# Performance work log

Hardware: AMD Instinct MI355X
Metric: run time of the kernel (lower is better)

The kernel has to match this reference:

```python
import jax, jax.numpy as jnp
import numpy as np

B, D, G, P = 4, 768, 64, 256
H = 12
HD = D // H
SCALE = HD ** -0.5


def setup_inputs() -> dict:
    key = jax.random.key(0)
    k1, k2, k3, k4 = jax.random.split(key, 4)
    x = jax.random.normal(k1, (B, D, G, P), dtype=jnp.float32)
    # per-group patch-patch mask; p=0.9 keep so no row is fully masked in practice
    mask = jax.random.bernoulli(k2, 0.9, (G, P, P))
    w_qkv = jax.random.normal(k3, (3 * D, D), dtype=jnp.float32) * (D ** -0.5)
    w_proj = jax.random.normal(k4, (D, D), dtype=jnp.float32) * (D ** -0.5)
    b_proj = jnp.zeros((D,), dtype=jnp.float32)
    return {"x": x, "mask": mask, "w_qkv": w_qkv, "w_proj": w_proj, "b_proj": b_proj}


def reference(x, mask, w_qkv, w_proj, b_proj):
    # 1x1 conv == channel matmul: [B,D,G,P] -> [B,3D,G,P]
    qkv = jnp.einsum('bdgp,ed->begp', x, w_qkv)
    # channel layout is (qkv, head, head_dim)
    qkv = qkv.reshape(B, 3, H, HD, G, P)
    qkv = jnp.transpose(qkv, (1, 0, 2, 4, 5, 3))  # [3, B, H, G, P, HD]
    q, k, v = qkv[0], qkv[1], qkv[2]
    attn = jnp.einsum('bhgpd,bhgqd->bhgpq', q, k) * SCALE  # [B,H,G,P,P]
    mask_value = -jnp.finfo(attn.dtype).max
    attn = jnp.where(mask[None, None], attn, mask_value)
    attn = jax.nn.softmax(attn, axis=-1)
    out = jnp.einsum('bhgpq,bhgqd->bhgpd', attn, v)  # [B,H,G,P,HD]
    out = jnp.transpose(out, (0, 1, 4, 2, 3)).reshape(B, D, G, P)
    out = jnp.einsum('bdgp,ed->begp', out, w_proj) + b_proj[None, :, None, None]
    return out
```

## Files before the change

### kernel.cpp

```cpp
#include <hip/hip_runtime.h>
#include <float.h>

#define D_    768
#define GD    64
#define PD    256
#define HH    12
#define HDD   64
#define NGP   (GD*PD)
#define SCALE 0.125f

typedef __bf16 bf16x8 __attribute__((ext_vector_type(8)));
typedef __bf16 bf16x4 __attribute__((ext_vector_type(4)));
typedef _Float16 f16x8 __attribute__((ext_vector_type(8)));
typedef _Float16 f16x4 __attribute__((ext_vector_type(4)));
typedef float  f32x4  __attribute__((ext_vector_type(4)));

__device__ __forceinline__ void gload_lds16(const __bf16* g, __bf16* l) {
  __builtin_amdgcn_global_load_lds(
      (const __attribute__((address_space(1))) void*)g,
      (__attribute__((address_space(3))) void*)l, 16, 0, 0);
}

__device__ __forceinline__ unsigned short f2bf_bits(float f) {
  __bf16 h = (__bf16)f;
  unsigned short u;
  __builtin_memcpy(&u, &h, 2);
  return u;
}

__global__ void wcast_k(const float* __restrict__ in, __bf16* __restrict__ out, int n) {
  int i = (blockIdx.x * 256 + threadIdx.x) * 4;
  if (i >= n) return;
  float4 v = *(const float4*)(in + i);
  bf16x4 o;
  o[0] = (__bf16)v.x; o[1] = (__bf16)v.y; o[2] = (__bf16)v.z; o[3] = (__bf16)v.w;
  *(bf16x4*)(out + i) = o;
}

__global__ void tcast_k(const float* __restrict__ in, __bf16* __restrict__ out) {
  __shared__ float s[32][66];
  const int tid = threadIdx.x;
  const int c0 = blockIdx.x * 64;
  const int r0 = blockIdx.y * 32;
  const int lx = tid & 63, ly = tid >> 6;
  #pragma unroll
  for (int rr = 0; rr < 32; rr += 4)
    s[rr + ly][lx] = in[(size_t)(r0 + rr + ly) * NGP + c0 + lx];
  __syncthreads();
  const int wx = tid & 15, wy = tid >> 4;
  unsigned* outu = (unsigned*)out;
  #pragma unroll
  for (int p = 0; p < 64; p += 16) {
    int j = p + wy;
    unsigned pk = (unsigned)f2bf_bits(s[2*wx][j]) |
                  ((unsigned)f2bf_bits(s[2*wx+1][j]) << 16);
    outu[(size_t)(c0 + j) * (D_/2) + (r0 >> 1) + wx] = pk;
  }
}

template<int BIAS, int OUT>
__global__ __launch_bounds__(256, 2)
void mfma_gemm(const __bf16* __restrict__ A, const __bf16* __restrict__ Bt,
               const float* __restrict__ bias, void* __restrict__ Cout,
               int M, int N, int K) {
  __shared__ __align__(16) __bf16 As[128 * 32];
  __shared__ __align__(16) __bf16 Bs[128 * 32];
  const int tid = threadIdx.x;
  const int wave = tid >> 6, lane = tid & 63;
  const int wm = wave >> 1, wn = wave & 1;
  const int m0 = blockIdx.y * 128, n0 = blockIdx.x * 128;

  const int r0g = wave * 2, r1g = wave * 2 + 1;
  const int kch = (lane >> 4) * 8;
  const __bf16* gA0 = A  + (size_t)(m0 + r0g * 16 + (lane & 15)) * K + kch;
  const __bf16* gA1 = gA0 + (size_t)16 * K;
  const __bf16* gB0 = Bt + (size_t)(n0 + r0g * 16 + (lane & 15)) * K + kch;
  const __bf16* gB1 = gB0 + (size_t)16 * K;
  __bf16* lA0 = As + r0g * 512;  __bf16* lA1 = As + r1g * 512;
  __bf16* lB0 = Bs + r0g * 512;  __bf16* lB1 = Bs + r1g * 512;

  f32x4 acc[4][4] = {};
  const bf16x8* Av = (const bf16x8*)As;
  const bf16x8* Bv = (const bf16x8*)Bs;

  for (int k0 = 0; k0 < K; k0 += 32) {
    __syncthreads();
    gload_lds16(gA0, lA0); gload_lds16(gA1, lA1);
    gload_lds16(gB0, lB0); gload_lds16(gB1, lB1);
    gA0 += 32; gA1 += 32; gB0 += 32; gB1 += 32;
    __syncthreads();
    bf16x8 af[4], bf[4];
    #pragma unroll
    for (int i = 0; i < 4; ++i) af[i] = Av[(wm * 4 + i) * 64 + lane];
    #pragma unroll
    for (int j = 0; j < 4; ++j) bf[j] = Bv[(wn * 4 + j) * 64 + lane];
    #pragma unroll
    for (int i = 0; i < 4; ++i)
      #pragma unroll
      for (int j = 0; j < 4; ++j)
        acc[i][j] = __builtin_amdgcn_mfma_f32_16x16x32_bf16(af[i], bf[j], acc[i][j], 0, 0, 0);
  }

  #pragma unroll
  for (int i = 0; i < 4; ++i) {
    #pragma unroll
    for (int j = 0; j < 4; ++j) {
      const int col  = n0 + wn * 64 + j * 16 + (lane & 15);
      const int row0 = m0 + wm * 64 + i * 16 + (lane >> 4) * 4;
      #pragma unroll
      for (int r = 0; r < 4; ++r) {
        float v = acc[i][j][r];
        if (BIAS) v += bias[row0 + r];
        if (OUT == 1)
          ((__bf16*)Cout)[(size_t)(row0 + r) * N + col] = (__bf16)v;
        else if (OUT == 2)
          ((_Float16*)Cout)[(size_t)(row0 + r) * N + col] = (_Float16)v;
        else
          ((float*)Cout)[(size_t)(row0 + r) * N + col] = v;
      }
    }
  }
}

__global__ __launch_bounds__(256, 2)
void attn_mfma(const __bf16* __restrict__ qkT, const _Float16* __restrict__ vbuf,
               const unsigned char* __restrict__ mask, __bf16* __restrict__ aot) {
  __shared__ unsigned mb[256][8];
  __shared__ __align__(16) _Float16 p_lds[4][4096];

  const int g = blockIdx.x, h = blockIdx.y;
  const int tid = threadIdx.x;
  const int wave = tid >> 6, lane = tid & 63;
  const int l15 = lane & 15, t4 = lane >> 4;

  const __bf16* qbase = qkT + (size_t)(g*PD + wave*64 + l15) * 1536 + h*HDD + t4*8;
  bf16x8 qf[4][2];
  #pragma unroll
  for (int j = 0; j < 4; ++j)
    #pragma unroll
    for (int ks = 0; ks < 2; ++ks)
      qf[j][ks] = *(const bf16x8*)(qbase + (size_t)j*16*1536 + ks*32);

  const unsigned* mwords = (const unsigned*)mask;
  bool is_i32 = true;
  #pragma unroll
  for (int i = 0; i < 16; ++i) is_i32 = is_i32 && (mwords[i] <= 1u);
  if (is_i32) {
    const uint4* mr4 = (const uint4*)(mwords + ((size_t)g*PD + tid)*PD);
    #pragma unroll
    for (int w = 0; w < 8; ++w) {
      unsigned bits = 0;
      #pragma unroll
      for (int j = 0; j < 8; ++j) {
        uint4 m4 = mr4[w*8 + j];
        bits |= (m4.x ? 1u : 0u) << (j*4+0);
        bits |= (m4.y ? 1u : 0u) << (j*4+1);
        bits |= (m4.z ? 1u : 0u) << (j*4+2);
        bits |= (m4.w ? 1u : 0u) << (j*4+3);
      }
      mb[tid][w] = bits;
    }
  } else {
    const unsigned* mr = (const unsigned*)(mask + ((size_t)g*PD + tid)*PD);
    #pragma unroll
    for (int w = 0; w < 8; ++w) {
      unsigned bits = 0;
      #pragma unroll
      for (int j = 0; j < 8; ++j) {
        unsigned vv = mr[w*8 + j];
        if (vv & 0x000000FFu) bits |= 1u << (j*4+0);
        if (vv & 0x0000FF00u) bits |= 1u << (j*4+1);
        if (vv & 0x00FF0000u) bits |= 1u << (j*4+2);
        if (vv & 0xFF000000u) bits |= 1u << (j*4+3);
      }
      mb[tid][w] = bits;
    }
  }
  __syncthreads();

  const __bf16* kbase = qkT + (size_t)(g*PD + l15) * 1536 + D_ + h*HDD + t4*8;
  const _Float16* vb  = vbuf + (size_t)(h*HDD + l15) * NGP + g*PD + t4*8;
  _Float16* pw = &p_lds[wave][0];

  float rm[4], rl[4];
  #pragma unroll
  for (int j = 0; j < 4; ++j) { rm[j] = -1e30f; rl[j] = 0.f; }
  f32x4 o[4][4] = {};

  for (int qt = 0; qt < 4; ++qt) {
    bf16x8 kf[4][2];
    #pragma unroll
    for (int i = 0; i < 4; ++i)
      #pragma unroll
      for (int ks = 0; ks < 2; ++ks)
        kf[i][ks] = *(const bf16x8*)(kbase + (size_t)(qt*64 + i*16)*1536 + ks*32);
    f32x4 s[4][4] = {};
    #pragma unroll
    for (int ks = 0; ks < 2; ++ks)
      #pragma unroll
      for (int i = 0; i < 4; ++i)
        #pragma unroll
        for (int j = 0; j < 4; ++j)
          s[i][j] = __builtin_amdgcn_mfma_f32_16x16x32_bf16(kf[i][ks], qf[j][ks], s[i][j], 0, 0, 0);

    #pragma unroll
    for (int j = 0; j < 4; ++j) {
      const int pl = wave*64 + j*16 + l15;
      const unsigned w0 = mb[pl][qt*2 + 0], w1 = mb[pl][qt*2 + 1];
      float mxj = -1e30f;
      #pragma unroll
      for (int i = 0; i < 4; ++i) {
        const unsigned w = (i < 2) ? w0 : w1;
        const int base = (i & 1)*16 + t4*4;
        #pragma unroll
        for (int r = 0; r < 4; ++r) {
          float sv = ((w >> (base + r)) & 1u) ? s[i][j][r] : -1e30f;
          s[i][j][r] = sv;
          mxj = fmaxf(mxj, sv);
        }
      }
      mxj = fmaxf(mxj, __shfl_xor(mxj, 16, 64));
      mxj = fmaxf(mxj, __shfl_xor(mxj, 32, 64));
      const float mnew = fmaxf(rm[j], mxj);
      const float scl  = __expf((rm[j] - mnew) * SCALE);
      const float mneg = -mnew * SCALE;
      rm[j] = mnew;
      float rs = 0.f;
      #pragma unroll
      for (int i = 0; i < 4; ++i)
        #pragma unroll
        for (int r = 0; r < 4; ++r) {
          float e = __expf(fmaf(s[i][j][r], SCALE, mneg));
          s[i][j][r] = e;
          rs += e;
        }
      rs += __shfl_xor(rs, 16, 64);
      rs += __shfl_xor(rs, 32, 64);
      rl[j] = fmaf(rl[j], scl, rs);
      #pragma unroll
      for (int i2 = 0; i2 < 4; ++i2)
        #pragma unroll
        for (int r = 0; r < 4; ++r)
          o[i2][j][r] *= scl;
      #pragma unroll
      for (int i = 0; i < 4; ++i) {
        f16x4 pk;
        #pragma unroll
        for (int r = 0; r < 4; ++r) pk[r] = (_Float16)s[i][j][r];
        *(f16x4*)&pw[j*1024 + (2*i + (t4 >> 1))*128 + l15*8 + 4*(t4 & 1)] = pk;
      }
    }

    f16x8 vf[4][2], pf[4][2];
    #pragma unroll
    for (int i2 = 0; i2 < 4; ++i2)
      #pragma unroll
      for (int ks = 0; ks < 2; ++ks)
        vf[i2][ks] = *(const f16x8*)(vb + (size_t)i2*16*NGP + qt*64 + ks*32);
    #pragma unroll
    for (int j2 = 0; j2 < 4; ++j2)
      #pragma unroll
      for (int ks = 0; ks < 2; ++ks)
        pf[j2][ks] = *(const f16x8*)&pw[j2*1024 + (4*ks + t4)*128 + l15*8];
    #pragma unroll
    for (int ks = 0; ks < 2; ++ks)
      #pragma unroll
      for (int i2 = 0; i2 < 4; ++i2)
        #pragma unroll
        for (int j2 = 0; j2 < 4; ++j2)
          o[i2][j2] = __builtin_amdgcn_mfma_f32_16x16x32_f16(vf[i2][ks], pf[j2][ks], o[i2][j2], 0, 0, 0);
  }

  #pragma unroll
  for (int j2 = 0; j2 < 4; ++j2) {
    const float inv = 1.f / rl[j2];
    __bf16* ao = aot + (size_t)(g*PD + wave*64 + j2*16 + l15) * D_ + h*HDD;
    #pragma unroll
    for (int i2 = 0; i2 < 4; ++i2) {
      bf16x4 ov;
      #pragma unroll
      for (int r = 0; r < 4; ++r) ov[r] = (__bf16)(o[i2][j2][r] * inv);
      *(bf16x4*)(ao + i2*16 + t4*4) = ov;
    }
  }
}

extern "C" void kernel_launch(void* const* d_in, const int* in_sizes, int n_in,
                              void* d_out, int out_size, void* d_ws, size_t ws_size,
                              hipStream_t stream) {
  const float* x      = (const float*)d_in[0];
  const unsigned char* mask = (const unsigned char*)d_in[1];
  const float* w_qkv  = (const float*)d_in[2];
  const float* w_proj = (const float*)d_in[3];
  const float* b_proj = (const float*)d_in[4];
  float* out = (float*)d_out;

  char* ws = (char*)d_ws;
  __bf16*   qkT  = (__bf16*)ws;    ws += (size_t)NGP * 1536 * 2;
  _Float16* vf16 = (_Float16*)ws;  ws += (size_t)D_ * NGP * 2;
  __bf16*   xt   = (__bf16*)ws;    ws += (size_t)NGP * D_ * 2;
  __bf16*   aot  = (__bf16*)ws;    ws += (size_t)NGP * D_ * 2;
  __bf16*   wq_bf= (__bf16*)ws;    ws += (size_t)3 * D_ * D_ * 2;
  __bf16*   wp_bf= (__bf16*)ws;

  wcast_k<<<(3*D_*D_)/1024, 256, 0, stream>>>(w_qkv,  wq_bf, 3*D_*D_);
  wcast_k<<<(D_*D_)/1024,   256, 0, stream>>>(w_proj, wp_bf, D_*D_);

  for (int b = 0; b < 4; ++b) {
    const float* xb = x + (size_t)b * D_ * NGP;
    float* ob = out + (size_t)b * D_ * NGP;
    tcast_k<<<dim3(NGP/64, D_/32), 256, 0, stream>>>(xb, xt);
    mfma_gemm<0,1><<<dim3(1536/128, NGP/128), 256, 0, stream>>>(xt, wq_bf, nullptr, qkT, NGP, 1536, D_);
    mfma_gemm<0,2><<<dim3(NGP/128, D_/128), 256, 0, stream>>>(wq_bf + (size_t)1536*D_, xt, nullptr, vf16, D_, NGP, D_);
    attn_mfma<<<dim3(GD, HH), 256, 0, stream>>>(qkT, vf16, mask, aot);
    mfma_gemm<1,0><<<dim3(NGP/128, D_/128), 256, 0, stream>>>(wp_bf, aot, b_proj, ob, D_, NGP, D_);
  }
}
```

Baseline: 1.223 ms.

## Batch all kernels across B, fold scale into Wq, lazy softmax rescale

When the workspace is large enough, the per-batch launch loop is replaced with single launches over all four batches. This gives the GEMM and attention kernels larger grids and cuts launch overhead, and the projection GEMM writes the output in batch layout directly. The softmax scale and log2e are folded into the Q weights so the kernel can use exp2. Rescaling of the running max is skipped when the new max is within a threshold, and the V loads are hoisted ahead of the softmax to overlap their latency. The risks are that the batched path needs about 4x the workspace and only runs when ws_size allows it, and that the deferred rescale lets exponentials reach up to 2^8, which narrows the fp16 margin for P.

```diff
diff --git a/kernel.cpp b/kernel.cpp
--- a/kernel.cpp
+++ b/kernel.cpp
@@ -7,7 +7,9 @@
 #define HH    12
 #define HDD   64
 #define NGP   (GD*PD)
+#define NB    4
 #define SCALE 0.125f
+#define QPRE  (0.125f * 1.44269504f)
 
 typedef __bf16 bf16x8 __attribute__((ext_vector_type(8)));
 typedef __bf16 bf16x4 __attribute__((ext_vector_type(4)));
@@ -15,6 +17,10 @@
 typedef _Float16 f16x4 __attribute__((ext_vector_type(4)));
 typedef float  f32x4  __attribute__((ext_vector_type(4)));
 
+__device__ __forceinline__ float exp2_fast(float x) {
+  return __builtin_amdgcn_exp2f(x);
+}
+
 __device__ __forceinline__ void gload_lds16(const __bf16* g, __bf16* l) {
   __builtin_amdgcn_global_load_lds(
       (const __attribute__((address_space(1))) void*)g,
@@ -28,12 +34,15 @@
   return u;
 }
 
-__global__ void wcast_k(const float* __restrict__ in, __bf16* __restrict__ out, int n) {
+__global__ void wcast_k(const float* __restrict__ in, __bf16* __restrict__ out, int n,
+                        int nscale, float sc) {
   int i = (blockIdx.x * 256 + threadIdx.x) * 4;
   if (i >= n) return;
+  float s = (i < nscale) ? sc : 1.f;
   float4 v = *(const float4*)(in + i);
   bf16x4 o;
-  o[0] = (__bf16)v.x; o[1] = (__bf16)v.y; o[2] = (__bf16)v.z; o[3] = (__bf16)v.w;
+  o[0] = (__bf16)(v.x * s); o[1] = (__bf16)(v.y * s);
+  o[2] = (__bf16)(v.z * s); o[3] = (__bf16)(v.w * s);
   *(bf16x4*)(out + i) = o;
 }
 
@@ -42,13 +51,14 @@
   const int tid = threadIdx.x;
   const int c0 = blockIdx.x * 64;
   const int r0 = blockIdx.y * 32;
+  const float* inz = in + (size_t)blockIdx.z * D_ * NGP;
+  unsigned* outu = (unsigned*)out + (size_t)blockIdx.z * NGP * (D_ / 2);
   const int lx = tid & 63, ly = tid >> 6;
   #pragma unroll
   for (int rr = 0; rr < 32; rr += 4)
-    s[rr + ly][lx] = in[(size_t)(r0 + rr + ly) * NGP + c0 + lx];
+    s[rr + ly][lx] = inz[(size_t)(r0 + rr + ly) * NGP + c0 + lx];
   __syncthreads();
   const int wx = tid & 15, wy = tid >> 4;
-  unsigned* outu = (unsigned*)out;
   #pragma unroll
   for (int p = 0; p < 64; p += 16) {
     int j = p + wy;
@@ -58,7 +68,7 @@
   }
 }
 
-template<int BIAS, int OUT>
+template<int BIAS, int OUT, int OUTB>
 __global__ __launch_bounds__(256, 2)
 void mfma_gemm(const __bf16* __restrict__ A, const __bf16* __restrict__ Bt,
                const float* __restrict__ bias, void* __restrict__ Cout,
@@ -115,7 +125,10 @@
           ((__bf16*)Cout)[(size_t)(row0 + r) * N + col] = (__bf16)v;
         else if (OUT == 2)
           ((_Float16*)Cout)[(size_t)(row0 + r) * N + col] = (_Float16)v;
-        else
+        else if (OUTB) {
+          const int bb = col >> 14, gp = col & (NGP - 1);
+          ((float*)Cout)[((size_t)bb * D_ + row0 + r) * NGP + gp] = v;
+        } else
           ((float*)Cout)[(size_t)(row0 + r) * N + col] = v;
       }
     }
@@ -124,16 +137,19 @@
 
 __global__ __launch_bounds__(256, 2)
 void attn_mfma(const __bf16* __restrict__ qkT, const _Float16* __restrict__ vbuf,
-               const unsigned char* __restrict__ mask, __bf16* __restrict__ aot) {
-  __shared__ unsigned mb[256][8];
+               const unsigned char* __restrict__ mask, __bf16* __restrict__ aot,
+               int vcols) {
+  __shared__ unsigned mb[256][9];
   __shared__ __align__(16) _Float16 p_lds[4][4096];
 
-  const int g = blockIdx.x, h = blockIdx.y;
+  const int g = blockIdx.x, h = blockIdx.y, b = blockIdx.z;
   const int tid = threadIdx.x;
   const int wave = tid >> 6, lane = tid & 63;
   const int l15 = lane & 15, t4 = lane >> 4;
 
-  const __bf16* qbase = qkT + (size_t)(g*PD + wave*64 + l15) * 1536 + h*HDD + t4*8;
+  const __bf16* qk = qkT + (size_t)b * NGP * 1536;
+
+  const __bf16* qbase = qk + (size_t)(g*PD + wave*64 + l15) * 1536 + h*HDD + t4*8;
   bf16x8 qf[4][2];
   #pragma unroll
   for (int j = 0; j < 4; ++j)
@@ -178,8 +194,8 @@
   }
   __syncthreads();
 
-  const __bf16* kbase = qkT + (size_t)(g*PD + l15) * 1536 + D_ + h*HDD + t4*8;
-  const _Float16* vb  = vbuf + (size_t)(h*HDD + l15) * NGP + g*PD + t4*8;
+  const __bf16* kbase = qk + (size_t)(g*PD + l15) * 1536 + D_ + h*HDD + t4*8;
+  const _Float16* vb  = vbuf + (size_t)(h*HDD + l15) * vcols + (size_t)b*NGP + g*PD + t4*8;
   _Float16* pw = &p_lds[wave][0];
 
   float rm[4], rl[4];
@@ -202,6 +218,13 @@
         #pragma unroll
         for (int j = 0; j < 4; ++j)
           s[i][j] = __builtin_amdgcn_mfma_f32_16x16x32_bf16(kf[i][ks], qf[j][ks], s[i][j], 0, 0, 0);
+
+    f16x8 vf[4][2];
+    #pragma unroll
+    for (int i2 = 0; i2 < 4; ++i2)
+      #pragma unroll
+      for (int ks = 0; ks < 2; ++ks)
+        vf[i2][ks] = *(const f16x8*)(vb + (size_t)i2*16*vcols + qt*64 + ks*32);
 
     #pragma unroll
     for (int j = 0; j < 4; ++j) {
@@ -221,27 +244,32 @@
       }
       mxj = fmaxf(mxj, __shfl_xor(mxj, 16, 64));
       mxj = fmaxf(mxj, __shfl_xor(mxj, 32, 64));
-      const float mnew = fmaxf(rm[j], mxj);
-      const float scl  = __expf((rm[j] - mnew) * SCALE);
-      const float mneg = -mnew * SCALE;
-      rm[j] = mnew;
+      const bool defer = __all(mxj <= rm[j] + 8.f);
+      const float mnew = defer ? rm[j] : fmaxf(rm[j], mxj);
+      const float mneg = -mnew;
       float rs = 0.f;
       #pragma unroll
       for (int i = 0; i < 4; ++i)
         #pragma unroll
         for (int r = 0; r < 4; ++r) {
-          float e = __expf(fmaf(s[i][j][r], SCALE, mneg));
+          float e = exp2_fast(s[i][j][r] + mneg);
           s[i][j][r] = e;
           rs += e;
         }
       rs += __shfl_xor(rs, 16, 64);
       rs += __shfl_xor(rs, 32, 64);
-      rl[j] = fmaf(rl[j], scl, rs);
-      #pragma unroll
-      for (int i2 = 0; i2 < 4; ++i2)
-        #pragma unroll
-        for (int r = 0; r < 4; ++r)
-          o[i2][j][r] *= scl;
+      if (defer) {
+        rl[j] += rs;
+      } else {
+        const float scl = exp2_fast(rm[j] - mnew);
+        rl[j] = fmaf(rl[j], scl, rs);
+        #pragma unroll
+        for (int i2 = 0; i2 < 4; ++i2)
+          #pragma unroll
+          for (int r = 0; r < 4; ++r)
+            o[i2][j][r] *= scl;
+        rm[j] = mnew;
+      }
       #pragma unroll
       for (int i = 0; i < 4; ++i) {
         f16x4 pk;
@@ -251,12 +279,7 @@
       }
     }
 
-    f16x8 vf[4][2], pf[4][2];
-    #pragma unroll
-    for (int i2 = 0; i2 < 4; ++i2)
-      #pragma unroll
-      for (int ks = 0; ks < 2; ++ks)
-        vf[i2][ks] = *(const f16x8*)(vb + (size_t)i2*16*NGP + qt*64 + ks*32);
+    f16x8 pf[4][2];
     #pragma unroll
     for (int j2 = 0; j2 < 4; ++j2)
       #pragma unroll
@@ -274,7 +297,7 @@
   #pragma unroll
   for (int j2 = 0; j2 < 4; ++j2) {
     const float inv = 1.f / rl[j2];
-    __bf16* ao = aot + (size_t)(g*PD + wave*64 + j2*16 + l15) * D_ + h*HDD;
+    __bf16* ao = aot + ((size_t)b*NGP + g*PD + wave*64 + j2*16 + l15) * D_ + h*HDD;
     #pragma unroll
     for (int i2 = 0; i2 < 4; ++i2) {
       bf16x4 ov;
@@ -295,24 +318,43 @@
   const float* b_proj = (const float*)d_in[4];
   float* out = (float*)d_out;
 
+  const size_t sz_qkT = (size_t)NB * NGP * 1536 * 2;
+  const size_t sz_v   = (size_t)D_ * NB * NGP * 2;
+  const size_t sz_xt  = (size_t)NB * NGP * D_ * 2;
+  const size_t sz_aot = (size_t)NB * NGP * D_ * 2;
+  const size_t sz_wq  = (size_t)3 * D_ * D_ * 2;
+  const size_t sz_wp  = (size_t)D_ * D_ * 2;
+  const size_t need_big = sz_qkT + sz_v + sz_xt + sz_aot + sz_wq + sz_wp;
+
+  const bool big = ws_size >= need_big;
+
   char* ws = (char*)d_ws;
-  __bf16*   qkT  = (__bf16*)ws;    ws += (size_t)NGP * 1536 * 2;
-  _Float16* vf16 = (_Float16*)ws;  ws += (size_t)D_ * NGP * 2;
-  __bf16*   xt   = (__bf16*)ws;    ws += (size_t)NGP * D_ * 2;
-  __bf16*   aot  = (__bf16*)ws;    ws += (size_t)NGP * D_ * 2;
-  __bf16*   wq_bf= (__bf16*)ws;    ws += (size_t)3 * D_ * D_ * 2;
+  __bf16*   qkT  = (__bf16*)ws;    ws += big ? sz_qkT : (size_t)NGP*1536*2;
+  _Float16* vf16 = (_Float16*)ws;  ws += big ? sz_v   : (size_t)D_*NGP*2;
+  __bf16*   xt   = (__bf16*)ws;    ws += big ? sz_xt  : (size_t)NGP*D_*2;
+  __bf16*   aot  = (__bf16*)ws;    ws += big ? sz_aot : (size_t)NGP*D_*2;
+  __bf16*   wq_bf= (__bf16*)ws;    ws += sz_wq;
   __bf16*   wp_bf= (__bf16*)ws;
 
-  wcast_k<<<(3*D_*D_)/1024, 256, 0, stream>>>(w_qkv,  wq_bf, 3*D_*D_);
-  wcast_k<<<(D_*D_)/1024,   256, 0, stream>>>(w_proj, wp_bf, D_*D_);
-
-  for (int b = 0; b < 4; ++b) {
-    const float* xb = x + (size_t)b * D_ * NGP;
-    float* ob = out + (size_t)b * D_ * NGP;
-    tcast_k<<<dim3(NGP/64, D_/32), 256, 0, stream>>>(xb, xt);
-    mfma_gemm<0,1><<<dim3(1536/128, NGP/128), 256, 0, stream>>>(xt, wq_bf, nullptr, qkT, NGP, 1536, D_);
-    mfma_gemm<0,2><<<dim3(NGP/128, D_/128), 256, 0, stream>>>(wq_bf + (size_t)1536*D_, xt, nullptr, vf16, D_, NGP, D_);
-    attn_mfma<<<dim3(GD, HH), 256, 0, stream>>>(qkT, vf16, mask, aot);
-    mfma_gemm<1,0><<<dim3(NGP/128, D_/128), 256, 0, stream>>>(wp_bf, aot, b_proj, ob, D_, NGP, D_);
-  }
-}
+  wcast_k<<<(3*D_*D_)/1024, 256, 0, stream>>>(w_qkv,  wq_bf, 3*D_*D_, D_*D_, QPRE);
+  wcast_k<<<(D_*D_)/1024,   256, 0, stream>>>(w_proj, wp_bf, D_*D_, 0, 1.f);
+
+  if (big) {
+    const int NCOL = NB * NGP;
+    tcast_k<<<dim3(NGP/64, D_/32, NB), 256, 0, stream>>>(x, xt);
+    mfma_gemm<0,1,0><<<dim3(1536/128, NCOL/128), 256, 0, stream>>>(xt, wq_bf, nullptr, qkT, NCOL, 1536, D_);
+    mfma_gemm<0,2,0><<<dim3(NCOL/128, D_/128), 256, 0, stream>>>(wq_bf + (size_t)1536*D_, xt, nullptr, vf16, D_, NCOL, D_);
+    attn_mfma<<<dim3(GD, HH, NB), 256, 0, stream>>>(qkT, vf16, mask, aot, NCOL);
+    mfma_gemm<1,0,1><<<dim3(NCOL/128, D_/128), 256, 0, stream>>>(wp_bf, aot, b_proj, out, D_, NCOL, D_);
+  } else {
+    for (int b = 0; b < NB; ++b) {
+      const float* xb = x + (size_t)b * D_ * NGP;
+      float* ob = out + (size_t)b * D_ * NGP;
+      tcast_k<<<dim3(NGP/64, D_/32, 1), 256, 0, stream>>>(xb, xt);
+      mfma_gemm<0,1,0><<<dim3(1536/128, NGP/128), 256, 0, stream>>>(xt, wq_bf, nullptr, qkT, NGP, 1536, D_);
+      mfma_gemm<0,2,0><<<dim3(NGP/128, D_/128), 256, 0, stream>>>(wq_bf + (size_t)1536*D_, xt, nullptr, vf16, D_, NGP, D_);
+      attn_mfma<<<dim3(GD, HH, 1), 256, 0, stream>>>(qkT, vf16, mask, aot, NGP);
+      mfma_gemm<1,0,0><<<dim3(NGP/128, D_/128), 256, 0, stream>>>(wp_bf, aot, b_proj, ob, D_, NGP, D_);
+    }
+  }
+}
```

New measurement: 1.183 ms. -3.3%, faster.
